# Performance work log

Hardware: AMD Instinct MI355X
Metric: run time of the kernel (lower is better)

## Reference

```python
import jax, jax.numpy as jnp
import numpy as np
from jax import lax

B, C, H, W = 32, 32, 64, 64
K = 1024
DN_T = ('NCHW', 'IOHW', 'NCHW')  # conv_transpose: kernel [in, out, kh, kw]
DN_C = ('NCHW', 'OIHW', 'NCHW')  # conv:           kernel [out, in, kh, kw]


def setup_inputs() -> dict:
    key = jax.random.key(0)
    ks = jax.random.split(key, 8)
    return {
        'z': jax.random.normal(ks[0], (B, C, H, W), jnp.float32),
        'codebook': jax.random.normal(ks[1], (K, C), jnp.float32),
        'w1': jax.random.normal(ks[2], (32, 128, 4, 4), jnp.float32) * 0.05,
        'b1': jnp.zeros((128,), jnp.float32),
        'w2': jax.random.normal(ks[3], (128, 64, 4, 4), jnp.float32) * 0.05,
        'b2': jnp.zeros((64,), jnp.float32),
        'w3': jax.random.normal(ks[4], (3, 64, 3, 3), jnp.float32) * 0.05,
        'b3': jnp.zeros((3,), jnp.float32),
    }


def _quantize(z, codebook):
    # z: [B, C, H, W] -> flat [N, C]
    zf = jnp.transpose(z, (0, 2, 3, 1)).reshape(-1, z.shape[1])
    # squared distances: ||z||^2 - 2 z.E^T + ||E||^2  -> [N, K]
    d = (jnp.sum(zf * zf, axis=1, keepdims=True)
         - 2.0 * zf @ codebook.T
         + jnp.sum(codebook * codebook, axis=1))
    idx = jnp.argmin(d, axis=1)                      # [N]
    q = codebook[idx].reshape(z.shape[0], z.shape[2], z.shape[3], z.shape[1])
    q = jnp.transpose(q, (0, 3, 1, 2))               # [B, C, H, W]
    # straight-through estimator
    return z + lax.stop_gradient(q - z)


def _decode(q, w1, b1, w2, b2, w3, b3):
    x = lax.conv_transpose(q, w1, strides=(2, 2), padding='SAME',
                           dimension_numbers=DN_T) + b1[None, :, None, None]
    x = jax.nn.relu(x)                               # [B, 128, 2H, 2W]
    x = lax.conv_transpose(x, w2, strides=(2, 2), padding='SAME',
                           dimension_numbers=DN_T) + b2[None, :, None, None]
    x = jax.nn.relu(x)                               # [B, 64, 4H, 4W]
    x = lax.conv_general_dilated(x, w3, window_strides=(1, 1), padding='SAME',
                                 dimension_numbers=DN_C) + b3[None, :, None, None]
    return jax.nn.sigmoid(x)                         # [B, 3, 4H, 4W]


def reference(z, codebook, w1, b1, w2, b2, w3, b3):
    q = _quantize(z, codebook)
    return _decode(q, w1, b1, w2, b2, w3, b3)
```

## Files before the change

kernel.cpp:

```cpp
#include <hip/hip_runtime.h>
#include <hip/hip_bf16.h>


typedef __attribute__((ext_vector_type(8)))  short  bf16x8;
typedef __attribute__((ext_vector_type(4)))  float  f32x4;
typedef __attribute__((ext_vector_type(16))) float  f32x16;

static constexpr int B_=32, C_=32, H_=64, W_=64, K_=1024;
static constexpr int NPOS = B_*H_*W_;

__device__ __forceinline__ unsigned short f2bf(float f){
  unsigned u = __float_as_uint(f);
  u = u + 0x7FFFu + ((u>>16)&1u);
  return (unsigned short)(u>>16);
}
__device__ __forceinline__ float bf2f(unsigned short h){
  return __uint_as_float(((unsigned)h)<<16);
}
__device__ __forceinline__ f32x16 mfma32(bf16x8 a, bf16x8 b, f32x16 c){
  return __builtin_amdgcn_mfma_f32_32x32x16_bf16(a,b,c,0,0,0);
}
__device__ __forceinline__ f32x4 mfma16(bf16x8 a, bf16x8 b, f32x4 c){
  return __builtin_amdgcn_mfma_f32_16x16x32_bf16(a,b,c,0,0,0);
}
__device__ __forceinline__ void gload16(const void* g, void* l){
  __builtin_amdgcn_global_load_lds(
      (const __attribute__((address_space(1))) void*)(unsigned long long)g,
      (__attribute__((address_space(3))) void*)(unsigned)(unsigned long long)l,
      16, 0, 0);
}
#define WAITVM(N) asm volatile("s_waitcnt vmcnt(" #N ")" ::: "memory")
__device__ __forceinline__ void barrier_raw(){
  asm volatile("" ::: "memory");
  __builtin_amdgcn_s_barrier();
  asm volatile("" ::: "memory");
}

__global__ __launch_bounds__(256) void prep_kernel(
    const float* __restrict__ cb, const float* __restrict__ w1,
    const float* __restrict__ w2, const float* __restrict__ w3,
    double* __restrict__ cb64, double* __restrict__ e2,
    unsigned short* __restrict__ cbp_hi, unsigned short* __restrict__ cbp_lo,
    float* __restrict__ e2h,
    unsigned short* __restrict__ wt1p, unsigned short* __restrict__ wt2p,
    unsigned short* __restrict__ w3p, float* __restrict__ zpage,
    int* __restrict__ cnt) {
  int idx = blockIdx.x*256 + threadIdx.x;
  if (idx == 0) cnt[0] = 0;
  if (idx < 64) zpage[idx] = 0.f;
  if (idx < K_*C_) {
    float v = cb[idx];
    cb64[idx] = (double)v;
    unsigned short h = f2bf(v);
    cbp_hi[idx] = h;
    cbp_lo[idx] = f2bf(v - bf2f(h));
  }
  if (idx < K_) {
    double s = 0.0;
    #pragma unroll
    for (int c=0;c<C_;++c){ double v=(double)cb[idx*C_+c]; s+=v*v; }
    e2[idx] = s;
    e2h[idx] = -0.5f * (float)s;
  }
  if (idx < 65536) {
    int e=idx&7, lane=(idx>>3)&63, g=(idx>>9)&3, t=(idx>>11)&3, c=(idx>>13)&1, p=idx>>14;
    int ic = c*16 + (lane>>5)*8 + e;
    int oc = g*32 + (lane&31);
    int ky = 2*(t>>1) + (p>>1), kx = 2*(t&1) + (p&1);
    wt1p[idx] = f2bf(w1[((ic*128+oc)*4+ky)*4+kx]);
  }
  if (idx < 131072) {
    int e=idx&7, lane=(idx>>3)&63, g=(idx>>9)&1, t=(idx>>10)&3, c=(idx>>12)&3, m=(idx>>14)&1, p=idx>>15;
    int ic = m*64 + c*16 + (lane>>5)*8 + e;
    int oc = g*32 + (lane&31);
    int ky = 2*(t>>1) + (p>>1), kx = 2*(t&1) + (p&1);
    wt2p[idx] = f2bf(w2[((ic*64+oc)*4+ky)*4+kx]);
  }
  if (idx < 9216) {
    int e=idx&7, lane=(idx>>3)&63, c=(idx>>9)&1, t=idx>>10;
    int ic = c*32 + ((lane>>4)&3)*8 + e;
    int oc = lane&15;
    int dy = t/3, dx = t - 3*dy;
    w3p[idx] = (oc<3) ? f2bf(w3[((oc*64+ic)*3+dy)*3+dx]) : (unsigned short)0;
  }
}

__global__ __launch_bounds__(256) void zprep_kernel(
    const float* __restrict__ z, unsigned short* __restrict__ zth,
    unsigned short* __restrict__ ztl) {
  int n = blockIdx.x*256 + threadIdx.x;
  int b = n >> 12, hw = n & 4095;
  const float* zp = z + (((size_t)b*C_) << 12) + hw;
  unsigned short th[C_], tl[C_];
  #pragma unroll
  for (int c=0;c<C_;++c) {
    float v = zp[(size_t)c<<12];
    unsigned short h = f2bf(v);
    th[c] = h;
    tl[c] = f2bf(v - bf2f(h));
  }
  bf16x8* dh = (bf16x8*)(zth + (size_t)n*C_);
  bf16x8* dl = (bf16x8*)(ztl + (size_t)n*C_);
  #pragma unroll
  for (int v=0;v<4;++v){ dh[v]=((bf16x8*)th)[v]; dl[v]=((bf16x8*)tl)[v]; }
}

__global__ __launch_bounds__(256) void quantm_kernel(
    const unsigned short* __restrict__ zth, const unsigned short* __restrict__ ztl,
    const unsigned short* __restrict__ cbp_hi, const unsigned short* __restrict__ cbp_lo,
    const float* __restrict__ e2h, const float* __restrict__ cb,
    unsigned short* __restrict__ q, int* __restrict__ cnt, int* __restrict__ list) {
  __shared__ bf16x8 ch[1024], cl[1024];
  __shared__ float  el[256];
  int tid = threadIdx.x, lane = tid&63, wv = tid>>6;
  int m0 = blockIdx.x*128 + wv*32;
  int colL = lane&15, g = lane>>4;

  bf16x8 ah[2], al[2];
  #pragma unroll
  for (int mt=0;mt<2;++mt) {
    int pos = m0 + mt*16 + colL;
    ah[mt] = *(const bf16x8*)(zth + (size_t)pos*C_ + g*8);
    al[mt] = *(const bf16x8*)(ztl + (size_t)pos*C_ + g*8);
  }

  float b1[2][4], b2[2][4]; int i1[2][4];
  #pragma unroll
  for (int mt=0;mt<2;++mt)
    #pragma unroll
    for (int r=0;r<4;++r){ b1[mt][r]=-3e38f; b2[mt][r]=-3e38f; i1[mt][r]=0; }

  for (int cb0 = 0; cb0 < K_; cb0 += 256) {
    __syncthreads();
    {
      const bf16x8* sh = (const bf16x8*)cbp_hi + cb0*4;
      const bf16x8* sl = (const bf16x8*)cbp_lo + cb0*4;
      #pragma unroll
      for (int v=0;v<4;++v){ ch[tid + v*256] = sh[tid + v*256];
                             cl[tid + v*256] = sl[tid + v*256]; }
      el[tid] = e2h[cb0 + tid];
    }
    __syncthreads();
    #pragma unroll
    for (int nt=0; nt<16; ++nt) {
      int cloc = nt*16 + colL;
      float ei = el[cloc];
      bf16x8 bh = ch[cloc*4 + g];
      bf16x8 bl = cl[cloc*4 + g];
      int nidx = cb0 + cloc;
      #pragma unroll
      for (int mt=0;mt<2;++mt) {
        f32x4 acc = {ei, ei, ei, ei};
        acc = mfma16(al[mt], bh, acc);
        acc = mfma16(ah[mt], bl, acc);
        acc = mfma16(ah[mt], bh, acc);
        #pragma unroll
        for (int r=0;r<4;++r) {
          float s = acc[r];
          b2[mt][r] = fmaxf(b2[mt][r], fminf(s, b1[mt][r]));
          if (s > b1[mt][r]) { b1[mt][r] = s; i1[mt][r] = nidx; }
        }
      }
    }
  }

  #pragma unroll
  for (int mask=1; mask<16; mask<<=1) {
    #pragma unroll
    for (int mt=0;mt<2;++mt)
      #pragma unroll
      for (int r=0;r<4;++r) {
        float o1 = __shfl_xor(b1[mt][r], mask);
        float o2 = __shfl_xor(b2[mt][r], mask);
        int   oi = __shfl_xor(i1[mt][r], mask);
        float nb2 = fmaxf(fminf(b1[mt][r], o1), fmaxf(b2[mt][r], o2));
        if (o1 > b1[mt][r]) { b1[mt][r] = o1; i1[mt][r] = oi; }
        b2[mt][r] = nb2;
      }
  }

  #pragma unroll
  for (int mt=0;mt<2;++mt)
    #pragma unroll
    for (int r=0;r<4;++r) {
      int m = m0 + mt*16 + g*4 + r;
      int idx = i1[mt][r];
      unsigned h0 = f2bf(cb[idx*C_ + 2*colL]);
      unsigned h1 = f2bf(cb[idx*C_ + 2*colL + 1]);
      ((unsigned*)q)[(((size_t)(colL>>2))*NPOS + m)*4 + (colL&3)] = h0 | (h1<<16);
      if (colL == 0 && (b1[mt][r] - b2[mt][r]) < 0.02f) {
        int slot = atomicAdd(cnt, 1);
        list[slot] = m;
      }
    }
}

__global__ __launch_bounds__(256) void refine_kernel(
    const int* __restrict__ cnt, const int* __restrict__ list,
    const float* __restrict__ z, const double* __restrict__ cb64,
    const double* __restrict__ e2, const float* __restrict__ cb,
    unsigned short* __restrict__ q) {
  __shared__ double lcb[64*33];
  __shared__ double le2[64];
  int tid = threadIdx.x, lane = tid&63, wv = tid>>6;
  int n_ref = cnt[0];
  int stride = (int)gridDim.x * 4;
  for (int base = 0; base < n_ref; base += stride) {
    int widx = base + (int)blockIdx.x*4 + wv;
    bool active = widx < n_ref;
    int m = active ? list[widx] : 0;
    double zr[C_];
    if (active) {
      int b = m >> 12, hw = m & 4095;
      const float* zp = z + (((size_t)b*C_) << 12) + hw;
      #pragma unroll
      for (int c=0;c<C_;++c) zr[c] = (double)zp[(size_t)c<<12];
    }
    double best = -1e300; int bi = 0;
    for (int ck = 0; ck < 16; ++ck) {
      __syncthreads();
      {
        const double* src = cb64 + (size_t)ck*2048 + (size_t)tid*8;
        int row = tid >> 2, col = (tid & 3)*8;
        #pragma unroll
        for (int j=0;j<8;++j) lcb[row*33 + col + j] = src[j];
        if (tid < 64) le2[tid] = e2[ck*64 + tid];
      }
      __syncthreads();
      if (active) {
        const double* e = &lcb[lane*33];
        double a0=0,a1=0,a2=0,a3=0;
        #pragma unroll
        for (int c=0;c<C_;c+=4) {
          a0 += zr[c  ]*e[c  ]; a1 += zr[c+1]*e[c+1];
          a2 += zr[c+2]*e[c+2]; a3 += zr[c+3]*e[c+3];
        }
        double s = 2.0*((a0+a1)+(a2+a3)) - le2[lane];
        if (s > best) { best = s; bi = ck*64 + lane; }
      }
    }
    #pragma unroll
    for (int mask=1; mask<64; mask<<=1) {
      double ob = __shfl_xor(best, mask);
      int    oi = __shfl_xor(bi, mask);
      if (ob > best || (ob == best && oi < bi)) { best = ob; bi = oi; }
    }
    if (active && lane < 16) {
      unsigned h0 = f2bf(cb[bi*C_ + 2*lane]);
      unsigned h1 = f2bf(cb[bi*C_ + 2*lane + 1]);
      ((unsigned*)q)[(((size_t)(lane>>2))*NPOS + m)*4 + (lane&3)] = h0 | (h1<<16);
    }
  }
}

__global__ __launch_bounds__(256) void convt1_kernel(
    const unsigned short* __restrict__ q, const unsigned short* __restrict__ wt1p,
    const float* __restrict__ b1, const float* __restrict__ zpage,
    unsigned short* __restrict__ x1, int b0) {
  __shared__ unsigned short At[4*4*34*8];
  int tid = threadIdx.x;
  int p = tid>>6, py=(tid>>7)&1, px=(tid>>6)&1;
  int lane = tid&63, xi = lane&31, half = lane>>5, ocl = lane&31;
  int bl = blockIdx.z, b = b0 + bl;
  int Y0 = blockIdx.y*2, X0 = blockIdx.x*32;

  for (int s = tid; s < 544; s += 256) {
    int t = (s*1928)>>16;
    int c = s - t*34;
    int r = t & 3, k8 = t >> 2;
    int hg = Y0-1+r, wg = X0-1+c;
    const unsigned short* src =
        (hg>=0 && hg<64 && wg>=0 && wg<64)
            ? q + ((size_t)k8*NPOS + ((b<<12) + hg*64 + wg))*8
            : (const unsigned short*)zpage;
    *(bf16x8*)&At[s*8] = *(const bf16x8*)src;
  }
  __syncthreads();

  f32x16 acc[2][4];
  #pragma unroll
  for (int g=0;g<4;++g){
    float bv = b1[g*32+ocl];
    #pragma unroll
    for (int yr=0;yr<2;++yr){
      #pragma unroll
      for (int r=0;r<16;++r) acc[yr][g][r]=bv;
    }
  }

  #pragma unroll
  for (int c16=0;c16<2;++c16) {
    #pragma unroll
    for (int t=0;t<4;++t) {
      int j=t>>1, kx=t&1;
      int col = xi+px+kx;
      int rb = (c16*2+half)*4 + py + j;
      bf16x8 a0 = *(const bf16x8*)&At[((rb+0)*34+col)*8];
      bf16x8 a1 = *(const bf16x8*)&At[((rb+1)*34+col)*8];
      const unsigned short* wb = wt1p + ((size_t)(((p*2+c16)*4+t)*4)*64 + lane)*8;
      #pragma unroll
      for (int g=0;g<4;++g) {
        bf16x8 bf = *(const bf16x8*)(wb + g*512);
        acc[0][g] = mfma32(a0, bf, acc[0][g]);
        acc[1][g] = mfma32(a1, bf, acc[1][g]);
      }
    }
  }

  #pragma unroll
  for (int yr=0;yr<2;++yr) {
    int Y = 2*(Y0+yr)+py;
    #pragma unroll
    for (int g=0;g<4;++g) {
      int oc = g*32 + ocl, cg = oc>>3, o8 = oc&7;
      unsigned short* dst = x1 + ((((size_t)bl*16 + cg)*128 + Y)*128 + (2*X0+px))*8 + o8;
      #pragma unroll
      for (int r=0;r<16;++r) {
        int xo = (r&3) + 8*(r>>2) + 4*half;
        dst[(size_t)xo*16] = f2bf(fmaxf(acc[yr][g][r], 0.f));
      }
    }
  }
}

__global__ __launch_bounds__(512, 4) void convt2_kernel(
    const unsigned short* __restrict__ x1, const unsigned short* __restrict__ wt2p,
    const float* __restrict__ b2, const float* __restrict__ zpage,
    unsigned short* __restrict__ x2) {
  __shared__ unsigned short At[4*1024*8];
  int tid = threadIdx.x;
  int wv = __builtin_amdgcn_readfirstlane(tid>>6);
  int lane = tid&63;
  int p = wv>>1, yh = wv&1;
  int py = p>>1, px = p&1;
  int xi = lane&31, half = lane>>5, ocl = lane&31;
  int bl = blockIdx.z;
  int Y0 = blockIdx.y*4, X0 = blockIdx.x*32;

  auto issue = [&](int P) {
    int m = P>>1, h = P&1;
    const unsigned short* xsrc = x1 + ((size_t)bl*16 + m*8 + h*4)*128*128*8;
    #pragma unroll
    for (int it = 0; it < 2; ++it) {
      int u0 = it*512 + wv*64;
      int u = u0 + lane;
      int tl = (u*1928)>>16;
      int c  = u - tl*34;
      int k8 = (tl*43)>>8;
      int r  = tl - k8*6;
      int hg = Y0-1+r, wg = X0-1+c;
      bool v = (u < 816) && hg>=0 && hg<128 && wg>=0 && wg<128;
      const void* src = v ? (const void*)(xsrc + (((size_t)k8*128 + hg)*128 + wg)*8)
                          : (const void*)zpage;
      gload16(src, (void*)&At[((size_t)P*1024 + u0)*8]);
    }
  };

  f32x16 acc[2][2];
  #pragma unroll
  for (int g=0;g<2;++g){
    float bv = b2[g*32+ocl];
    #pragma unroll
    for (int yr=0;yr<2;++yr)
      #pragma unroll
      for (int r=0;r<16;++r) acc[yr][g][r]=bv;
  }

  auto compute = [&](int P) {
    int m = P>>1;
    const unsigned short* Ab = &At[(size_t)P*1024*8];
    __builtin_amdgcn_s_setprio(1);
    #pragma unroll
    for (int ci=0; ci<2; ++ci) {
      int c16 = (P&1)*2 + ci;
      #pragma unroll
      for (int t=0;t<4;++t) {
        int j=t>>1, kx=t&1;
        int col = xi+px+kx;
        int lrow = ((c16*2+half)&3)*6 + py + j + yh*2;
        bf16x8 a0 = *(const bf16x8*)&Ab[((lrow+0)*34+col)*8];
        bf16x8 a1 = *(const bf16x8*)&Ab[((lrow+1)*34+col)*8];
        const unsigned short* wb = wt2p + ((size_t)(((((p*2+m)*4+c16)*4+t)*2))*64 + lane)*8;
        bf16x8 bf0 = *(const bf16x8*)wb;
        bf16x8 bf1 = *(const bf16x8*)(wb + 512);
        acc[0][0]=mfma32(a0,bf0,acc[0][0]); acc[1][0]=mfma32(a1,bf0,acc[1][0]);
        acc[0][1]=mfma32(a0,bf1,acc[0][1]); acc[1][1]=mfma32(a1,bf1,acc[1][1]);
      }
    }
    __builtin_amdgcn_s_setprio(0);
  };

  issue(0); issue(1); issue(2);
  WAITVM(4); barrier_raw();
  compute(0);
  issue(3);
  WAITVM(4); barrier_raw();
  compute(1);
  WAITVM(2); barrier_raw();
  compute(2);
  WAITVM(0); barrier_raw();
  compute(3);

  #pragma unroll
  for (int yr=0;yr<2;++yr) {
    int Y = 2*(Y0 + yh*2 + yr) + py;
    #pragma unroll
    for (int g=0;g<2;++g) {
      int oc = g*32 + ocl, cg = oc>>3, o8 = oc&7;
      unsigned short* dst = x2 + ((((size_t)bl*8 + cg)*256 + Y)*256 + (2*X0+px))*8 + o8;
      #pragma unroll
      for (int r=0;r<16;++r) {
        int xo = (r&3) + 8*(r>>2) + 4*half;
        dst[(size_t)xo*16] = f2bf(fmaxf(acc[yr][g][r], 0.f));
      }
    }
  }
}

__global__ __launch_bounds__(512) void conv3_kernel(
    const unsigned short* __restrict__ x2, const unsigned short* __restrict__ w3p,
    const float* __restrict__ b3, const float* __restrict__ zpage,
    float* __restrict__ out, int b0) {
  __shared__ unsigned short Xt[2][1536*8];
  int tid = threadIdx.x, w = tid>>6, lane = tid&63;
  int xi = lane&15, k8A = (lane>>4)&3, oc = lane&15;
  int bl = blockIdx.z, b = b0 + bl;
  int y0 = blockIdx.y*8, x0 = blockIdx.x*32;
  int y = y0 + w;

  auto stage = [&](int c, int buf) {
    #pragma unroll
    for (int i=0;i<3;++i) {
      int sbase = i*512 + w*64;
      int s = sbase + lane;
      int t = (s*1928)>>16;
      int cc = s - t*34;
      int k8 = (t*26)>>8;
      int r = t - k8*10;
      int rf = y0-1+r, cf = x0-1+cc;
      bool ok = (s < 1360) && rf>=0 && rf<256 && cf>=0 && cf<256;
      const void* src = ok
          ? (const void*)(x2 + ((((size_t)bl*8 + c*4 + k8)*256 + rf)*256 + cf)*8)
          : (const void*)zpage;
      gload16(src, (void*)&Xt[buf][sbase*8]);
    }
  };

  f32x4 acc[2];
  float bv = (oc<3) ? b3[oc] : 0.f;
  acc[0][0]=bv; acc[0][1]=bv; acc[0][2]=bv; acc[0][3]=bv;
  acc[1][0]=bv; acc[1][1]=bv; acc[1][2]=bv; acc[1][3]=bv;

  auto compute = [&](int c, int buf) {
    #pragma unroll
    for (int t=0;t<9;++t) {
      int dy = t/3, dx = t - 3*dy;
      bf16x8 bf = *(const bf16x8*)(w3p + ((size_t)(t*2+c)*64 + lane)*8);
      #pragma unroll
      for (int mt=0;mt<2;++mt) {
        bf16x8 a = *(const bf16x8*)&Xt[buf][((size_t)(k8A*10 + (w+dy))*34 + (mt*16 + xi + dx))*8];
        acc[mt] = mfma16(a, bf, acc[mt]);
      }
    }
  };

  stage(0, 0);
  WAITVM(0); barrier_raw();
  stage(1, 1);
  compute(0, 0);
  WAITVM(0); barrier_raw();
  compute(1, 1);

  if (oc < 3) {
    #pragma unroll
    for (int mt=0;mt<2;++mt) {
      f32x4 v;
      #pragma unroll
      for (int r=0;r<4;++r) v[r] = 1.f/(1.f + __expf(-acc[mt][r]));
      int x = x0 + mt*16 + ((lane>>4)&3)*4;
      *(f32x4*)(out + (((size_t)b*3 + oc)*256 + y)*256 + x) = v;
    }
  }
}

extern "C" void kernel_launch(void* const* d_in, const int* in_sizes, int n_in,
                              void* d_out, int out_size, void* d_ws, size_t ws_size,
                              hipStream_t stream) {
  const float* z  = (const float*)d_in[0];
  const float* cb = (const float*)d_in[1];
  const float* w1 = (const float*)d_in[2];
  const float* b1 = (const float*)d_in[3];
  const float* w2 = (const float*)d_in[4];
  const float* b2 = (const float*)d_in[5];
  const float* w3 = (const float*)d_in[6];
  const float* b3 = (const float*)d_in[7];
  float* out = (float*)d_out;

  char* ws = (char*)d_ws;
  size_t off = 0;
  auto alloc = [&](size_t bytes) -> void* {
    void* p = (void*)(ws + off);
    off += (bytes + 255) & ~(size_t)255;
    return p;
  };
  double* cb64         = (double*)alloc((size_t)K_*C_*8);
  double* e2           = (double*)alloc((size_t)K_*8);
  float*  zpage        = (float*)alloc(256);
  unsigned short* cbph = (unsigned short*)alloc((size_t)K_*C_*2);
  unsigned short* cbpl = (unsigned short*)alloc((size_t)K_*C_*2);
  float*  e2h          = (float*)alloc((size_t)K_*4);
  int*    cnt          = (int*)alloc(256);
  int*    list         = (int*)alloc((size_t)NPOS*4);
  unsigned short* zth  = (unsigned short*)alloc((size_t)NPOS*C_*2);
  unsigned short* ztl  = (unsigned short*)alloc((size_t)NPOS*C_*2);
  unsigned short* wt1p = (unsigned short*)alloc((size_t)65536*2);
  unsigned short* wt2p = (unsigned short*)alloc((size_t)131072*2);
  unsigned short* w3p  = (unsigned short*)alloc((size_t)9216*2);
  unsigned short* q    = (unsigned short*)alloc((size_t)NPOS*C_*2);
  size_t fixed = off;

  size_t per_b = ((size_t)16*128*128*8 + (size_t)8*256*256*8) * 2;
  long long avail = (long long)ws_size - (long long)fixed;
  int chunk = (avail >= (long long)per_b) ? (int)(avail / (long long)per_b) : 1;
  if (chunk > B_) chunk = B_;
  if      (chunk >= 32) chunk = 32;
  else if (chunk >= 16) chunk = 16;
  else if (chunk >=  8) chunk =  8;
  else if (chunk >=  4) chunk =  4;
  else if (chunk >=  2) chunk =  2;
  else                  chunk =  1;
  unsigned short* x1 = (unsigned short*)alloc((size_t)chunk*16*128*128*8*2);
  unsigned short* x2 = (unsigned short*)alloc((size_t)chunk*8*256*256*8*2);

  prep_kernel<<<512, 256, 0, stream>>>(cb, w1, w2, w3, cb64, e2, cbph, cbpl,
                                       e2h, wt1p, wt2p, w3p, zpage, cnt);
  zprep_kernel<<<512, 256, 0, stream>>>(z, zth, ztl);
  quantm_kernel<<<1024, 256, 0, stream>>>(zth, ztl, cbph, cbpl, e2h, cb,
                                          q, cnt, list);
  refine_kernel<<<512, 256, 0, stream>>>(cnt, list, z, cb64, e2, cb, q);

  for (int b0 = 0; b0 < B_; b0 += chunk) {
    int nb = (B_ - b0 < chunk) ? (B_ - b0) : chunk;
    convt1_kernel<<<dim3(2,32,nb), 256, 0, stream>>>(q, wt1p, b1, zpage, x1, b0);
    convt2_kernel<<<dim3(4,32,nb), 512, 0, stream>>>(x1, wt2p, b2, zpage, x2);
    conv3_kernel <<<dim3(8,32,nb), 512, 0, stream>>>(x2, w3p, b3, zpage, out, b0);
  }
}
```

Measured before the change: 440.0 us.

## Halve convt2 row tile and split waves by output-channel group

The convt2 kernel now gives each block 2 input rows instead of 4, doubling the grid in y. Waves are now split by output-channel half rather than by row half, so each wave keeps 2 accumulators instead of 4. The LDS tile shrinks to 640 entries per stage, with a dummy destination for the excess loads, and launch bounds rise to 6 blocks per CU. The aim is higher occupancy and lower register and LDS pressure. The cost is more halo reloading per output, since each tile now carries 2 halo rows for only 2 output rows, plus more weight loads per MFMA.

After: 474.4 us. +7.8%, slower.

```diff
diff --git a/kernel.cpp b/kernel.cpp
--- a/kernel.cpp
+++ b/kernel.cpp
@@ -323,68 +323,71 @@
   }
 }
 
-__global__ __launch_bounds__(512, 4) void convt2_kernel(
+__global__ __launch_bounds__(512, 6) void convt2_kernel(
     const unsigned short* __restrict__ x1, const unsigned short* __restrict__ wt2p,
     const float* __restrict__ b2, const float* __restrict__ zpage,
     unsigned short* __restrict__ x2) {
-  __shared__ unsigned short At[4*1024*8];
+  __shared__ unsigned short At[(4*640 + 64)*8];
   int tid = threadIdx.x;
   int wv = __builtin_amdgcn_readfirstlane(tid>>6);
   int lane = tid&63;
-  int p = wv>>1, yh = wv&1;
+  int p = wv>>1, g = wv&1;
   int py = p>>1, px = p&1;
   int xi = lane&31, half = lane>>5, ocl = lane&31;
   int bl = blockIdx.z;
-  int Y0 = blockIdx.y*4, X0 = blockIdx.x*32;
+  int Y0 = blockIdx.y*2, X0 = blockIdx.x*32;
 
   auto issue = [&](int P) {
     int m = P>>1, h = P&1;
     const unsigned short* xsrc = x1 + ((size_t)bl*16 + m*8 + h*4)*128*128*8;
     #pragma unroll
     for (int it = 0; it < 2; ++it) {
-      int u0 = it*512 + wv*64;
-      int u = u0 + lane;
-      int tl = (u*1928)>>16;
-      int c  = u - tl*34;
-      int k8 = (tl*43)>>8;
-      int r  = tl - k8*6;
+      int sbase = it*512 + wv*64;
+      bool realdst = (sbase < 576);
+      int s = sbase + lane;
+      int k8l = (s*482)>>16;
+      int rem = s - k8l*136;
+      int r = (rem*1928)>>16;
+      int c = rem - r*34;
       int hg = Y0-1+r, wg = X0-1+c;
-      bool v = (u < 816) && hg>=0 && hg<128 && wg>=0 && wg<128;
-      const void* src = v ? (const void*)(xsrc + (((size_t)k8*128 + hg)*128 + wg)*8)
+      bool v = (s < 544) && hg>=0 && hg<128 && wg>=0 && wg<128;
+      const void* src = v ? (const void*)(xsrc + (((size_t)k8l*128 + hg)*128 + wg)*8)
                           : (const void*)zpage;
-      gload16(src, (void*)&At[((size_t)P*1024 + u0)*8]);
+      void* dst = realdst ? (void*)&At[((size_t)P*640 + sbase)*8]
+                          : (void*)&At[(size_t)2560*8];
+      gload16(src, dst);
     }
   };
 
-  f32x16 acc[2][2];
-  #pragma unroll
-  for (int g=0;g<2;++g){
+  f32x16 acc[2];
+  {
     float bv = b2[g*32+ocl];
     #pragma unroll
     for (int yr=0;yr<2;++yr)
       #pragma unroll
-      for (int r=0;r<16;++r) acc[yr][g][r]=bv;
+      for (int r=0;r<16;++r) acc[yr][r]=bv;
   }
 
   auto compute = [&](int P) {
     int m = P>>1;
-    const unsigned short* Ab = &At[(size_t)P*1024*8];
+    const unsigned short* Ab = &At[(size_t)P*640*8];
     __builtin_amdgcn_s_setprio(1);
     #pragma unroll
     for (int ci=0; ci<2; ++ci) {
       int c16 = (P&1)*2 + ci;
+      int k8l = 2*ci + half;
       #pragma unroll
       for (int t=0;t<4;++t) {
         int j=t>>1, kx=t&1;
         int col = xi+px+kx;
-        int lrow = ((c16*2+half)&3)*6 + py + j + yh*2;
-        bf16x8 a0 = *(const bf16x8*)&Ab[((lrow+0)*34+col)*8];
-        bf16x8 a1 = *(const bf16x8*)&Ab[((lrow+1)*34+col)*8];
-        const unsigned short* wb = wt2p + ((size_t)(((((p*2+m)*4+c16)*4+t)*2))*64 + lane)*8;
-        bf16x8 bf0 = *(const bf16x8*)wb;
-        bf16x8 bf1 = *(const bf16x8*)(wb + 512);
-        acc[0][0]=mfma32(a0,bf0,acc[0][0]); acc[1][0]=mfma32(a1,bf0,acc[1][0]);
-        acc[0][1]=mfma32(a0,bf1,acc[0][1]); acc[1][1]=mfma32(a1,bf1,acc[1][1]);
+        int base = (k8l*4 + py + j)*34 + col;
+        bf16x8 a0 = *(const bf16x8*)&Ab[(base     )*8];
+        bf16x8 a1 = *(const bf16x8*)&Ab[(base + 34)*8];
+        const unsigned short* wb = wt2p +
+            ((size_t)(((((p*2+m)*4+c16)*4+t)*2) + g)*64 + lane)*8;
+        bf16x8 bf = *(const bf16x8*)wb;
+        acc[0] = mfma32(a0, bf, acc[0]);
+        acc[1] = mfma32(a1, bf, acc[1]);
       }
     }
     __builtin_amdgcn_s_setprio(0);
@@ -403,16 +406,13 @@
 
   #pragma unroll
   for (int yr=0;yr<2;++yr) {
-    int Y = 2*(Y0 + yh*2 + yr) + py;
-    #pragma unroll
-    for (int g=0;g<2;++g) {
-      int oc = g*32 + ocl, cg = oc>>3, o8 = oc&7;
-      unsigned short* dst = x2 + ((((size_t)bl*8 + cg)*256 + Y)*256 + (2*X0+px))*8 + o8;
-      #pragma unroll
-      for (int r=0;r<16;++r) {
-        int xo = (r&3) + 8*(r>>2) + 4*half;
-        dst[(size_t)xo*16] = f2bf(fmaxf(acc[yr][g][r], 0.f));
-      }
+    int Y = 2*(Y0 + yr) + py;
+    int oc = g*32 + ocl, cg = oc>>3, o8 = oc&7;
+    unsigned short* dst = x2 + ((((size_t)bl*8 + cg)*256 + Y)*256 + (2*X0+px))*8 + o8;
+    #pragma unroll
+    for (int r=0;r<16;++r) {
+      int xo = (r&3) + 8*(r>>2) + 4*half;
+      dst[(size_t)xo*16] = f2bf(fmaxf(acc[yr][r], 0.f));
     }
   }
 }
@@ -542,7 +542,7 @@
   for (int b0 = 0; b0 < B_; b0 += chunk) {
     int nb = (B_ - b0 < chunk) ? (B_ - b0) : chunk;
     convt1_kernel<<<dim3(2,32,nb), 256, 0, stream>>>(q, wt1p, b1, zpage, x1, b0);
-    convt2_kernel<<<dim3(4,32,nb), 512, 0, stream>>>(x1, wt2p, b2, zpage, x2);
+    convt2_kernel<<<dim3(4,64,nb), 512, 0, stream>>>(x1, wt2p, b2, zpage, x2);
     conv3_kernel <<<dim3(8,32,nb), 512, 0, stream>>>(x2, w3p, b3, zpage, out, b0);
   }
 }
```
